# Optimization experiments

Hardware: AMD Instinct MI355X
Metric: run time of the kernel (lower is better)

Reference implementation:

```python
import jax, jax.numpy as jnp
import numpy as np

N = 50000
E = 1600000
N_INPUT, N_ENC1, N_ENC2, N_ENC3, N_Z, N_CLUSTERS = 512, 500, 500, 2000, 10, 10
SIGMA = 0.5


def _xavier(key, shape):
    bound = float(np.sqrt(6.0 / (shape[0] + shape[1])))
    return jax.random.uniform(key, shape, jnp.float32, -bound, bound)


def setup_inputs() -> dict:
    key = jax.random.key(0)
    ks = jax.random.split(key, 13)
    x = jax.random.normal(ks[0], (N, N_INPUT), jnp.float32)
    tra1 = jax.random.normal(ks[1], (N, N_ENC1), jnp.float32)
    tra2 = jax.random.normal(ks[2], (N, N_ENC2), jnp.float32)
    tra3 = jax.random.normal(ks[3], (N, N_ENC3), jnp.float32)
    z = jax.random.normal(ks[4], (N, N_Z), jnp.float32)
    edge_vals = jax.random.uniform(ks[5], (E,), jnp.float32)
    row = jax.random.randint(ks[6], (E,), 0, N, jnp.int32)
    col = jax.random.randint(ks[7], (E,), 0, N, jnp.int32)
    W1 = _xavier(ks[8], (N_INPUT, N_ENC1))
    W2 = _xavier(ks[9], (N_ENC1, N_ENC2))
    W3 = _xavier(ks[10], (N_ENC2, N_ENC3))
    W4 = _xavier(ks[11], (N_ENC3, N_Z))
    W5 = _xavier(ks[12], (N_Z, N_CLUSTERS))
    return {"x": x, "tra1": tra1, "tra2": tra2, "tra3": tra3, "z": z,
            "edge_vals": edge_vals, "row": row, "col": col,
            "W1": W1, "W2": W2, "W3": W3, "W4": W4, "W5": W5}


def _spmm(row, col, vals, m):
    # out[i] = sum_{e: row[e]==i} vals[e] * m[col[e]]  (sparse adj @ m)
    return jax.ops.segment_sum(vals[:, None] * m[col], row, num_segments=N)


def _gnn_layer(feats, W, row, col, vals, active=True):
    out = _spmm(row, col, vals, feats @ W)
    return jax.nn.relu(out) if active else out


def reference(x, tra1, tra2, tra3, z, edge_vals, row, col, W1, W2, W3, W4, W5):
    s = SIGMA
    h = _gnn_layer(x, W1, row, col, edge_vals)
    h = _gnn_layer((1 - s) * h + s * tra1, W2, row, col, edge_vals)
    h = _gnn_layer((1 - s) * h + s * tra2, W3, row, col, edge_vals)
    h = _gnn_layer((1 - s) * h + s * tra3, W4, row, col, edge_vals)
    h = _gnn_layer((1 - s) * h + s * z, W5, row, col, edge_vals, active=False)
    return jax.nn.softmax(h, axis=1)
```

## Files before the change

### kernel.cpp

```cpp
#include <hip/hip_runtime.h>
#include <cstddef>
#include <cstdint>


constexpr int D_IN = 512;
constexpr int D1   = 500;
constexpr int D2   = 500;
constexpr int D3   = 2000;
constexpr int DC   = 10;

__global__ void zero_i32(int* __restrict__ p, int n) {
    int i = blockIdx.x * 256 + threadIdx.x;
    if (i < n) p[i] = 0;
}

__global__ void count_edges(const int* __restrict__ row, int E, int* __restrict__ cnt) {
    int e = blockIdx.x * 256 + threadIdx.x;
    if (e < E) atomicAdd(&cnt[row[e]], 1);
}

__global__ __launch_bounds__(1024) void scan_rowptr(const int* __restrict__ cnt, int Nr,
                                                    int* __restrict__ rp, int* __restrict__ cur) {
    __shared__ int sb[1024];
    const int t = threadIdx.x;
    int carry = 0;
    for (int base = 0; base < Nr; base += 1024) {
        int idx = base + t;
        int c = (idx < Nr) ? cnt[idx] : 0;
        sb[t] = c;
        __syncthreads();
        for (int off = 1; off < 1024; off <<= 1) {
            int add = (t >= off) ? sb[t - off] : 0;
            __syncthreads();
            sb[t] += add;
            __syncthreads();
        }
        if (idx < Nr) { int ex = carry + sb[t] - c; rp[idx] = ex; cur[idx] = ex; }
        carry += sb[1023];
        __syncthreads();
    }
    if (t == 0) rp[Nr] = carry;
}

__global__ void scatter_edges(const int* __restrict__ row, const int* __restrict__ col,
                              const float* __restrict__ val, int E,
                              int* __restrict__ cur, int* __restrict__ ci,
                              float* __restrict__ cv) {
    int e = blockIdx.x * 256 + threadIdx.x;
    if (e < E) {
        int r = row[e];
        int p = atomicAdd(&cur[r], 1);
        ci[p] = col[e];
        cv[p] = val[e];
    }
}

constexpr int BM = 64, BN = 64, BK = 16;

__global__ __launch_bounds__(256) void gemm_tiled(const float* __restrict__ A,
                                                  const float* __restrict__ B,
                                                  float* __restrict__ C,
                                                  int M, int K, int Nn) {
    __shared__ float As[BM][BK + 1];
    __shared__ float Bs[BK][BN];
    const int tid = threadIdx.x;
    const int tx = tid & 15, ty = tid >> 4;
    const int rowBase = blockIdx.y * BM, colBase = blockIdx.x * BN;
    float acc[4][4] = {};
    for (int k0 = 0; k0 < K; k0 += BK) {
        for (int e = tid; e < BM * BK; e += 256) {
            int m = e >> 4, k = e & 15;
            int gr = rowBase + m, gk = k0 + k;
            As[m][k] = (gr < M && gk < K) ? A[(size_t)gr * K + gk] : 0.f;
        }
        for (int e = tid; e < BK * BN; e += 256) {
            int k = e >> 6, n = e & 63;
            int gk = k0 + k, gc = colBase + n;
            Bs[k][n] = (gk < K && gc < Nn) ? B[(size_t)gk * Nn + gc] : 0.f;
        }
        __syncthreads();
        for (int k = 0; k < BK; k++) {
            float a[4], b[4];
#pragma unroll
            for (int i = 0; i < 4; i++) a[i] = As[ty * 4 + i][k];
#pragma unroll
            for (int j = 0; j < 4; j++) b[j] = Bs[k][tx * 4 + j];
#pragma unroll
            for (int i = 0; i < 4; i++)
#pragma unroll
                for (int j = 0; j < 4; j++) acc[i][j] += a[i] * b[j];
        }
        __syncthreads();
    }
#pragma unroll
    for (int i = 0; i < 4; i++) {
        int gr = rowBase + ty * 4 + i;
        if (gr >= M) continue;
#pragma unroll
        for (int j = 0; j < 4; j++) {
            int gc = colBase + tx * 4 + j;
            if (gc < Nn) C[(size_t)gr * Nn + gc] = acc[i][j];
        }
    }
}

constexpr int R3  = 20;
constexpr int JB  = 256;

__global__ __launch_bounds__(256, 3) void gemm34(const float* __restrict__ g3,
                                                 const float* __restrict__ W3,
                                                 const float* __restrict__ W4,
                                                 float* __restrict__ t4) {
    __shared__ float gs[R3 * D2];
    const int t = threadIdx.x;
    const size_t i0 = (size_t)blockIdx.x * R3;

    {
        const float4* src = reinterpret_cast<const float4*>(g3 + i0 * D2);
        float4* dst = reinterpret_cast<float4*>(gs);
        for (int e = t; e < R3 * D2 / 4; e += 256) dst[e] = src[e];
    }
    __syncthreads();

    const int lane = t & 63;
    const int rb = (t >> 6) * 5;
    float acc[5][10] = {};

    for (int j0 = 0; j0 < D3; j0 += JB) {
        const int jb = min(JB, D3 - j0);
        const int j4 = lane * 4;
        if (j4 < jb) {
            float pacc[5][4] = {};
            const float* w3p = W3 + j0 + j4;
            float4 wa[4], wb[4];

            auto load_w3 = [&](float4 (&dst)[4], int k) {
#pragma unroll
                for (int kk = 0; kk < 4; kk++)
                    dst[kk] = *reinterpret_cast<const float4*>(w3p + (k + kk) * D3);
            };
            auto fma_grp = [&](const float4 (&wv)[4], int k) {
                float4 ga[5];
#pragma unroll
                for (int i = 0; i < 5; i++)
                    ga[i] = *reinterpret_cast<const float4*>(&gs[(rb + i) * D2 + k]);
#pragma unroll
                for (int kk = 0; kk < 4; kk++)
#pragma unroll
                    for (int i = 0; i < 5; i++) {
                        const float av = reinterpret_cast<const float*>(&ga[i])[kk];
#pragma unroll
                        for (int jj = 0; jj < 4; jj++)
                            pacc[i][jj] += av * reinterpret_cast<const float*>(&wv[kk])[jj];
                    }
            };

            load_w3(wa, 0);
            for (int k = 0; k < D2 - 4; k += 8) {
                load_w3(wb, k + 4);
                fma_grp(wa, k);
                load_w3(wa, k + 8);
                fma_grp(wb, k + 4);
            }
            fma_grp(wa, D2 - 4);

#pragma unroll
            for (int jj = 0; jj < 4; jj++) {
                const float* w4r = W4 + (j0 + j4 + jj) * DC;
                float w4v[10];
#pragma unroll
                for (int h = 0; h < 5; h++) {
                    float2 u = *reinterpret_cast<const float2*>(w4r + 2 * h);
                    w4v[2 * h] = u.x;
                    w4v[2 * h + 1] = u.y;
                }
#pragma unroll
                for (int i = 0; i < 5; i++) {
                    const float p = fmaxf(pacc[i][jj], 0.f);
#pragma unroll
                    for (int c = 0; c < 10; c++) acc[i][c] += p * w4v[c];
                }
            }
        }
    }

#pragma unroll
    for (int i = 0; i < 5; i++)
#pragma unroll
        for (int c = 0; c < 10; c++) {
            float v = acc[i][c];
            v += __shfl_xor(v, 1, 64);
            v += __shfl_xor(v, 2, 64);
            v += __shfl_xor(v, 4, 64);
            v += __shfl_xor(v, 8, 64);
            v += __shfl_xor(v, 16, 64);
            v += __shfl_xor(v, 32, 64);
            acc[i][c] = v;
        }
    if (lane == 0) {
        float* dst = t4 + (i0 + rb) * DC;
#pragma unroll
        for (int i = 0; i < 5; i++)
#pragma unroll
            for (int c = 0; c < 10; c++) dst[i * DC + c] = 0.5f * acc[i][c];
    }
}

constexpr int RT = 16;

__global__ __launch_bounds__(256) void tra3w4(const float* __restrict__ tra3,
                                              const float* __restrict__ W4,
                                              float* __restrict__ t4) {
    const int t = threadIdx.x;
    const int r = t >> 4, l = t & 15;
    const size_t i = (size_t)blockIdx.x * RT + r;
    const float* rowp = tra3 + i * D3;
    float a[10] = {};
    for (int m = l; m < D3 / 4; m += 16) {
        float4 v = *reinterpret_cast<const float4*>(rowp + m * 4);
        const float* w4r = W4 + m * 4 * DC;
        const float vv[4] = {v.x, v.y, v.z, v.w};
#pragma unroll
        for (int q = 0; q < 4; q++)
#pragma unroll
            for (int c = 0; c < 10; c++) a[c] += vv[q] * w4r[q * DC + c];
    }
#pragma unroll
    for (int c = 0; c < 10; c++) {
        float v = a[c];
        v += __shfl_xor(v, 1, 64);
        v += __shfl_xor(v, 2, 64);
        v += __shfl_xor(v, 4, 64);
        v += __shfl_xor(v, 8, 64);
        a[c] = v;
    }
    if (l == 0) {
        float* dst = t4 + i * DC;
#pragma unroll
        for (int c = 0; c < 10; c++) dst[c] += 0.5f * a[c];
    }
}

__global__ __launch_bounds__(256) void spmm_w(const int* __restrict__ rp,
                                              const int* __restrict__ ci,
                                              const float* __restrict__ cv,
                                              const float* __restrict__ m,
                                              float* __restrict__ out,
                                              const float* __restrict__ mix,
                                              int relu) {
    const int i = blockIdx.x, t = threadIdx.x;
    const int c0 = t, c1 = t + 256;
    float a0 = 0.f, a1 = 0.f;
    const int pb = rp[i], pe = rp[i + 1];
    for (int p = pb; p < pe; p++) {
        const int col = ci[p];
        const float v = cv[p];
        const float* mr = m + (size_t)col * D1;
        a0 += v * mr[c0];
        if (c1 < D1) a1 += v * mr[c1];
    }
    if (relu) { a0 = fmaxf(a0, 0.f); a1 = fmaxf(a1, 0.f); }
    const size_t o = (size_t)i * D1;
    if (mix) {
        out[o + c0] = 0.5f * a0 + 0.5f * mix[o + c0];
        if (c1 < D1) out[o + c1] = 0.5f * a1 + 0.5f * mix[o + c1];
    } else {
        out[o + c0] = a0;
        if (c1 < D1) out[o + c1] = a1;
    }
}

__global__ __launch_bounds__(256) void spmm_n(const int* __restrict__ rp,
                                              const int* __restrict__ ci,
                                              const float* __restrict__ cv,
                                              const float* __restrict__ m,
                                              float* __restrict__ out,
                                              const float* __restrict__ mix,
                                              int relu, int Nr) {
    const int t = threadIdx.x;
    const int lr = t / DC, c = t - lr * DC;
    if (lr >= 25) return;
    const int i = blockIdx.x * 25 + lr;
    if (i >= Nr) return;
    float a = 0.f;
    const int pb = rp[i], pe = rp[i + 1];
    for (int p = pb; p < pe; p++) a += cv[p] * m[(size_t)ci[p] * DC + c];
    if (relu) a = fmaxf(a, 0.f);
    if (mix) a = 0.5f * a + 0.5f * mix[(size_t)i * DC + c];
    out[(size_t)i * DC + c] = a;
}

__global__ void softmax10(const float* __restrict__ in, float* __restrict__ out, int Nr) {
    int i = blockIdx.x * 256 + threadIdx.x;
    if (i >= Nr) return;
    const float* r = in + (size_t)i * DC;
    float v[DC], mx = r[0];
#pragma unroll
    for (int c = 0; c < DC; c++) { v[c] = r[c]; mx = fmaxf(mx, v[c]); }
    float s = 0.f;
#pragma unroll
    for (int c = 0; c < DC; c++) { v[c] = __expf(v[c] - mx); s += v[c]; }
    float inv = 1.0f / s;
    float* o = out + (size_t)i * DC;
#pragma unroll
    for (int c = 0; c < DC; c++) o[c] = v[c] * inv;
}

extern "C" void kernel_launch(void* const* d_in, const int* in_sizes, int n_in,
                              void* d_out, int out_size, void* d_ws, size_t ws_size,
                              hipStream_t stream) {
    const float* x    = (const float*)d_in[0];
    const float* tra1 = (const float*)d_in[1];
    const float* tra2 = (const float*)d_in[2];
    const float* tra3 = (const float*)d_in[3];
    const float* z    = (const float*)d_in[4];
    const float* ev   = (const float*)d_in[5];
    const int*   erow = (const int*)d_in[6];
    const int*   ecol = (const int*)d_in[7];
    const float* W1   = (const float*)d_in[8];
    const float* W2   = (const float*)d_in[9];
    const float* W3   = (const float*)d_in[10];
    const float* W4   = (const float*)d_in[11];
    const float* W5   = (const float*)d_in[12];

    const int Nr = in_sizes[4] / DC;
    const int E  = in_sizes[5];

    char* ws = (char*)d_ws;
    size_t off = 0;
    auto alloc = [&](size_t bytes) -> char* {
        char* p = ws + off;
        off = (off + bytes + 255) & ~(size_t)255;
        return p;
    };
    float* B0  = (float*)alloc((size_t)Nr * D1 * 4);
    float* B1  = (float*)alloc((size_t)Nr * D1 * 4);
    float* t4  = (float*)alloc((size_t)Nr * DC * 4);
    float* a4  = (float*)alloc((size_t)Nr * DC * 4);
    float* g5  = (float*)alloc((size_t)Nr * DC * 4);
    float* pre = (float*)alloc((size_t)Nr * DC * 4);
    int*   rp  = (int*)alloc((size_t)(Nr + 1) * 4);
    int*   cur = (int*)alloc((size_t)Nr * 4);
    int*   cnt = (int*)alloc((size_t)Nr * 4);
    int*   ci  = (int*)alloc((size_t)E * 4);
    float* cv  = (float*)alloc((size_t)E * 4);

    const int eb = (E + 255) / 256;
    const int nb = (Nr + 255) / 256;

    zero_i32<<<nb, 256, 0, stream>>>(cnt, Nr);
    count_edges<<<eb, 256, 0, stream>>>(erow, E, cnt);
    scan_rowptr<<<1, 1024, 0, stream>>>(cnt, Nr, rp, cur);
    scatter_edges<<<eb, 256, 0, stream>>>(erow, ecol, ev, E, cur, ci, cv);

    auto gg = [&](int M, int Nn) { return dim3((Nn + BN - 1) / BN, (M + BM - 1) / BM); };

    gemm_tiled<<<gg(Nr, D1), 256, 0, stream>>>(x, W1, B0, Nr, D_IN, D1);
    spmm_w<<<Nr, 256, 0, stream>>>(rp, ci, cv, B0, B1, tra1, 1);
    gemm_tiled<<<gg(Nr, D2), 256, 0, stream>>>(B1, W2, B0, Nr, D1, D2);
    spmm_w<<<Nr, 256, 0, stream>>>(rp, ci, cv, B0, B1, tra2, 1);
    spmm_w<<<Nr, 256, 0, stream>>>(rp, ci, cv, B1, B0, nullptr, 0);
    gemm34<<<Nr / R3, 256, 0, stream>>>(B0, W3, W4, t4);
    tra3w4<<<Nr / RT, 256, 0, stream>>>(tra3, W4, t4);
    spmm_n<<<(Nr + 24) / 25, 256, 0, stream>>>(rp, ci, cv, t4, a4, z, 1, Nr);
    gemm_tiled<<<gg(Nr, DC), 256, 0, stream>>>(a4, W5, g5, Nr, DC, DC);
    spmm_n<<<(Nr + 24) / 25, 256, 0, stream>>>(rp, ci, cv, g5, pre, nullptr, 0, Nr);
    softmax10<<<nb, 256, 0, stream>>>(pre, (float*)d_out, Nr);
}
```

Before: 5.438 ms.

## Replace tiled GEMMs with row-stripe GEMM staging weight k-slabs in shared memory

```diff
diff --git a/kernel.cpp b/kernel.cpp
--- a/kernel.cpp
+++ b/kernel.cpp
@@ -8,6 +8,9 @@
 constexpr int D2   = 500;
 constexpr int D3   = 2000;
 constexpr int DC   = 10;
+
+constexpr int RS = 32;
+constexpr int KG = 16;
 
 __global__ void zero_i32(int* __restrict__ p, int n) {
     int i = blockIdx.x * 256 + threadIdx.x;
@@ -55,154 +58,213 @@
     }
 }
 
-constexpr int BM = 64, BN = 64, BK = 16;
-
-__global__ __launch_bounds__(256) void gemm_tiled(const float* __restrict__ A,
-                                                  const float* __restrict__ B,
-                                                  float* __restrict__ C,
-                                                  int M, int K, int Nn) {
-    __shared__ float As[BM][BK + 1];
-    __shared__ float Bs[BK][BN];
-    const int tid = threadIdx.x;
-    const int tx = tid & 15, ty = tid >> 4;
-    const int rowBase = blockIdx.y * BM, colBase = blockIdx.x * BN;
-    float acc[4][4] = {};
-    for (int k0 = 0; k0 < K; k0 += BK) {
-        for (int e = tid; e < BM * BK; e += 256) {
-            int m = e >> 4, k = e & 15;
-            int gr = rowBase + m, gk = k0 + k;
-            As[m][k] = (gr < M && gk < K) ? A[(size_t)gr * K + gk] : 0.f;
-        }
-        for (int e = tid; e < BK * BN; e += 256) {
-            int k = e >> 6, n = e & 63;
-            int gk = k0 + k, gc = colBase + n;
-            Bs[k][n] = (gk < K && gc < Nn) ? B[(size_t)gk * Nn + gc] : 0.f;
+__global__ __launch_bounds__(256, 4) void gemm_stripe(const float* __restrict__ A,
+                                                      const float* __restrict__ B,
+                                                      float* __restrict__ C,
+                                                      int M, int K, int Nn,
+                                                      const float* __restrict__ zpad) {
+    __shared__ float Ws[KG][512];
+    const int t = threadIdx.x;
+    const int lane = t & 63;
+    const int wid = t >> 6;
+    const int i0 = blockIdx.x * RS;
+    const int rb = wid * 8;
+
+    const float* Ar[8];
+#pragma unroll
+    for (int i = 0; i < 8; i++) {
+        int rg = i0 + rb + i;
+        rg = rg < M ? rg : M - 1;
+        Ar[i] = A + (size_t)rg * K;
+    }
+
+    float pacc[8][8] = {};
+    const int ngroups = (K + KG - 1) / KG;
+
+    for (int g = 0; g < ngroups; g++) {
+        const int k0 = g * KG;
+        const int kg = min(KG, K - k0);
+        float4 st[8];
+#pragma unroll
+        for (int q = 0; q < 8; q++) {
+            int e = t + 256 * q;
+            int kk = e >> 7, jj4 = (e & 127) << 2;
+            const float* src = (kk < kg && jj4 < Nn)
+                                   ? (B + (size_t)(k0 + kk) * Nn + jj4)
+                                   : zpad;
+            st[q] = *reinterpret_cast<const float4*>(src);
         }
         __syncthreads();
-        for (int k = 0; k < BK; k++) {
-            float a[4], b[4];
-#pragma unroll
-            for (int i = 0; i < 4; i++) a[i] = As[ty * 4 + i][k];
-#pragma unroll
-            for (int j = 0; j < 4; j++) b[j] = Bs[k][tx * 4 + j];
-#pragma unroll
-            for (int i = 0; i < 4; i++)
-#pragma unroll
-                for (int j = 0; j < 4; j++) acc[i][j] += a[i] * b[j];
+#pragma unroll
+        for (int q = 0; q < 8; q++) {
+            int e = t + 256 * q;
+            int kk = e >> 7, jj4 = (e & 127) << 2;
+            *reinterpret_cast<float4*>(&Ws[kk][jj4]) = st[q];
         }
         __syncthreads();
-    }
-#pragma unroll
-    for (int i = 0; i < 4; i++) {
-        int gr = rowBase + ty * 4 + i;
-        if (gr >= M) continue;
-#pragma unroll
-        for (int j = 0; j < 4; j++) {
-            int gc = colBase + tx * 4 + j;
-            if (gc < Nn) C[(size_t)gr * Nn + gc] = acc[i][j];
-        }
-    }
-}
-
-constexpr int R3  = 20;
-constexpr int JB  = 256;
-
-__global__ __launch_bounds__(256, 3) void gemm34(const float* __restrict__ g3,
+        for (int k4 = 0; k4 < kg; k4 += 4) {
+            float4 ga[8];
+#pragma unroll
+            for (int i = 0; i < 8; i++)
+                ga[i] = *reinterpret_cast<const float4*>(Ar[i] + k0 + k4);
+#pragma unroll
+            for (int q = 0; q < 4; q++) {
+                float4 wlo = *reinterpret_cast<const float4*>(&Ws[k4 + q][4 * lane]);
+                float4 whi = *reinterpret_cast<const float4*>(&Ws[k4 + q][256 + 4 * lane]);
+#pragma unroll
+                for (int i = 0; i < 8; i++) {
+                    const float av = reinterpret_cast<const float*>(&ga[i])[q];
+                    pacc[i][0] += av * wlo.x;
+                    pacc[i][1] += av * wlo.y;
+                    pacc[i][2] += av * wlo.z;
+                    pacc[i][3] += av * wlo.w;
+                    pacc[i][4] += av * whi.x;
+                    pacc[i][5] += av * whi.y;
+                    pacc[i][6] += av * whi.z;
+                    pacc[i][7] += av * whi.w;
+                }
+            }
+        }
+    }
+#pragma unroll
+    for (int i = 0; i < 8; i++) {
+        int row = i0 + rb + i;
+        if (row >= M) break;
+        if (4 * lane + 4 <= Nn) {
+            float4 lo;
+            lo.x = pacc[i][0]; lo.y = pacc[i][1]; lo.z = pacc[i][2]; lo.w = pacc[i][3];
+            *reinterpret_cast<float4*>(C + (size_t)row * Nn + 4 * lane) = lo;
+        }
+        if (260 + 4 * lane <= Nn) {
+            float4 hi;
+            hi.x = pacc[i][4]; hi.y = pacc[i][5]; hi.z = pacc[i][6]; hi.w = pacc[i][7];
+            *reinterpret_cast<float4*>(C + (size_t)row * Nn + 256 + 4 * lane) = hi;
+        }
+    }
+}
+
+__global__ __launch_bounds__(256, 4) void gemm34(const float* __restrict__ g3,
                                                  const float* __restrict__ W3,
                                                  const float* __restrict__ W4,
-                                                 float* __restrict__ t4) {
-    __shared__ float gs[R3 * D2];
-    const int t = threadIdx.x;
-    const size_t i0 = (size_t)blockIdx.x * R3;
-
-    {
-        const float4* src = reinterpret_cast<const float4*>(g3 + i0 * D2);
-        float4* dst = reinterpret_cast<float4*>(gs);
-        for (int e = t; e < R3 * D2 / 4; e += 256) dst[e] = src[e];
-    }
-    __syncthreads();
-
+                                                 float* __restrict__ t4,
+                                                 int M, const float* __restrict__ zpad) {
+    __shared__ float Ws[KG][512];
+    const int t = threadIdx.x;
     const int lane = t & 63;
-    const int rb = (t >> 6) * 5;
-    float acc[5][10] = {};
-
-    for (int j0 = 0; j0 < D3; j0 += JB) {
-        const int jb = min(JB, D3 - j0);
-        const int j4 = lane * 4;
-        if (j4 < jb) {
-            float pacc[5][4] = {};
-            const float* w3p = W3 + j0 + j4;
-            float4 wa[4], wb[4];
-
-            auto load_w3 = [&](float4 (&dst)[4], int k) {
-#pragma unroll
-                for (int kk = 0; kk < 4; kk++)
-                    dst[kk] = *reinterpret_cast<const float4*>(w3p + (k + kk) * D3);
-            };
-            auto fma_grp = [&](const float4 (&wv)[4], int k) {
-                float4 ga[5];
-#pragma unroll
-                for (int i = 0; i < 5; i++)
-                    ga[i] = *reinterpret_cast<const float4*>(&gs[(rb + i) * D2 + k]);
-#pragma unroll
-                for (int kk = 0; kk < 4; kk++)
-#pragma unroll
-                    for (int i = 0; i < 5; i++) {
-                        const float av = reinterpret_cast<const float*>(&ga[i])[kk];
-#pragma unroll
-                        for (int jj = 0; jj < 4; jj++)
-                            pacc[i][jj] += av * reinterpret_cast<const float*>(&wv[kk])[jj];
+    const int wid = t >> 6;
+    const int i0 = blockIdx.x * RS;
+    const int rb = wid * 8;
+
+    const float* Ar[8];
+#pragma unroll
+    for (int i = 0; i < 8; i++) {
+        int rg = i0 + rb + i;
+        rg = rg < M ? rg : M - 1;
+        Ar[i] = g3 + (size_t)rg * D2;
+    }
+
+    for (int j0 = 0; j0 < D3; j0 += 512) {
+        float pacc[8][8] = {};
+        const int ngroups = (D2 + KG - 1) / KG;
+        for (int g = 0; g < ngroups; g++) {
+            const int k0 = g * KG;
+            const int kg = min(KG, D2 - k0);
+            float4 st[8];
+#pragma unroll
+            for (int q = 0; q < 8; q++) {
+                int e = t + 256 * q;
+                int kk = e >> 7, jj4 = (e & 127) << 2;
+                const float* src = (kk < kg && j0 + jj4 < D3)
+                                       ? (W3 + (size_t)(k0 + kk) * D3 + j0 + jj4)
+                                       : zpad;
+                st[q] = *reinterpret_cast<const float4*>(src);
+            }
+            __syncthreads();
+#pragma unroll
+            for (int q = 0; q < 8; q++) {
+                int e = t + 256 * q;
+                int kk = e >> 7, jj4 = (e & 127) << 2;
+                *reinterpret_cast<float4*>(&Ws[kk][jj4]) = st[q];
+            }
+            __syncthreads();
+            for (int k4 = 0; k4 < kg; k4 += 4) {
+                float4 ga[8];
+#pragma unroll
+                for (int i = 0; i < 8; i++)
+                    ga[i] = *reinterpret_cast<const float4*>(Ar[i] + k0 + k4);
+#pragma unroll
+                for (int q = 0; q < 4; q++) {
+                    float4 wlo = *reinterpret_cast<const float4*>(&Ws[k4 + q][4 * lane]);
+                    float4 whi = *reinterpret_cast<const float4*>(&Ws[k4 + q][256 + 4 * lane]);
+#pragma unroll
+                    for (int i = 0; i < 8; i++) {
+                        const float av = reinterpret_cast<const float*>(&ga[i])[q];
+                        pacc[i][0] += av * wlo.x;
+                        pacc[i][1] += av * wlo.y;
+                        pacc[i][2] += av * wlo.z;
+                        pacc[i][3] += av * wlo.w;
+                        pacc[i][4] += av * whi.x;
+                        pacc[i][5] += av * whi.y;
+                        pacc[i][6] += av * whi.z;
+                        pacc[i][7] += av * whi.w;
                     }
-            };
-
-            load_w3(wa, 0);
-            for (int k = 0; k < D2 - 4; k += 8) {
-                load_w3(wb, k + 4);
-                fma_grp(wa, k);
-                load_w3(wa, k + 8);
-                fma_grp(wb, k + 4);
-            }
-            fma_grp(wa, D2 - 4);
-
-#pragma unroll
-            for (int jj = 0; jj < 4; jj++) {
-                const float* w4r = W4 + (j0 + j4 + jj) * DC;
-                float w4v[10];
-#pragma unroll
-                for (int h = 0; h < 5; h++) {
-                    float2 u = *reinterpret_cast<const float2*>(w4r + 2 * h);
-                    w4v[2 * h] = u.x;
-                    w4v[2 * h + 1] = u.y;
                 }
-#pragma unroll
-                for (int i = 0; i < 5; i++) {
-                    const float p = fmaxf(pacc[i][jj], 0.f);
-#pragma unroll
-                    for (int c = 0; c < 10; c++) acc[i][c] += p * w4v[c];
+            }
+        }
+#pragma unroll
+        for (int h = 0; h < 2; h++) {
+            float ea[4][10] = {};
+#pragma unroll
+            for (int s = 0; s < 2; s++) {
+#pragma unroll
+                for (int jj = 0; jj < 4; jj++) {
+                    const int jc = j0 + s * 256 + 4 * lane + jj;
+                    float w4v[10];
+                    if (jc < D3) {
+                        const float* w4r = W4 + (size_t)jc * DC;
+#pragma unroll
+                        for (int u = 0; u < 5; u++) {
+                            float2 f = *reinterpret_cast<const float2*>(w4r + 2 * u);
+                            w4v[2 * u] = f.x;
+                            w4v[2 * u + 1] = f.y;
+                        }
+                    } else {
+#pragma unroll
+                        for (int c = 0; c < 10; c++) w4v[c] = 0.f;
+                    }
+#pragma unroll
+                    for (int i = 0; i < 4; i++) {
+                        const float p = fmaxf(pacc[h * 4 + i][s * 4 + jj], 0.f);
+#pragma unroll
+                        for (int c = 0; c < 10; c++) ea[i][c] += p * w4v[c];
+                    }
                 }
             }
-        }
-    }
-
-#pragma unroll
-    for (int i = 0; i < 5; i++)
-#pragma unroll
-        for (int c = 0; c < 10; c++) {
-            float v = acc[i][c];
-            v += __shfl_xor(v, 1, 64);
-            v += __shfl_xor(v, 2, 64);
-            v += __shfl_xor(v, 4, 64);
-            v += __shfl_xor(v, 8, 64);
-            v += __shfl_xor(v, 16, 64);
-            v += __shfl_xor(v, 32, 64);
-            acc[i][c] = v;
-        }
-    if (lane == 0) {
-        float* dst = t4 + (i0 + rb) * DC;
-#pragma unroll
-        for (int i = 0; i < 5; i++)
-#pragma unroll
-            for (int c = 0; c < 10; c++) dst[i * DC + c] = 0.5f * acc[i][c];
+#pragma unroll
+            for (int i = 0; i < 4; i++)
+#pragma unroll
+                for (int c = 0; c < 10; c++) {
+                    float v = ea[i][c];
+                    v += __shfl_xor(v, 1, 64);
+                    v += __shfl_xor(v, 2, 64);
+                    v += __shfl_xor(v, 4, 64);
+                    v += __shfl_xor(v, 8, 64);
+                    v += __shfl_xor(v, 16, 64);
+                    v += __shfl_xor(v, 32, 64);
+                    ea[i][c] = v;
+                }
+            if (lane == 0) {
+#pragma unroll
+                for (int i = 0; i < 4; i++) {
+                    const int row = i0 + rb + h * 4 + i;
+                    if (row < M) {
+                        float* dst = t4 + (size_t)row * DC;
+#pragma unroll
+                        for (int c = 0; c < 10; c++) dst[c] += 0.5f * ea[i][c];
+                    }
+                }
+            }
+        }
     }
 }
 
@@ -237,7 +299,39 @@
     if (l == 0) {
         float* dst = t4 + i * DC;
 #pragma unroll
-        for (int c = 0; c < 10; c++) dst[c] += 0.5f * a[c];
+        for (int c = 0; c < 10; c++) dst[c] = 0.5f * a[c];
+    }
+}
+
+__global__ __launch_bounds__(256) void gemm10(const float* __restrict__ a4,
+                                              const float* __restrict__ W5,
+                                              float* __restrict__ g5, int Nr) {
+    __shared__ float w5s[DC * DC];
+    const int t = threadIdx.x;
+    if (t < DC * DC) w5s[t] = W5[t];
+    __syncthreads();
+    const int i = blockIdx.x * 256 + t;
+    if (i >= Nr) return;
+    const float* ar = a4 + (size_t)i * DC;
+    float a[DC];
+#pragma unroll
+    for (int u = 0; u < 5; u++) {
+        float2 f = *reinterpret_cast<const float2*>(ar + 2 * u);
+        a[2 * u] = f.x;
+        a[2 * u + 1] = f.y;
+    }
+    float o[DC] = {};
+#pragma unroll
+    for (int k = 0; k < DC; k++)
+#pragma unroll
+        for (int c = 0; c < DC; c++) o[c] += a[k] * w5s[k * DC + c];
+    float* dst = g5 + (size_t)i * DC;
+#pragma unroll
+    for (int u = 0; u < 5; u++) {
+        float2 f;
+        f.x = o[2 * u];
+        f.y = o[2 * u + 1];
+        *reinterpret_cast<float2*>(dst + 2 * u) = f;
     }
 }
 
@@ -333,37 +427,39 @@
         off = (off + bytes + 255) & ~(size_t)255;
         return p;
     };
-    float* B0  = (float*)alloc((size_t)Nr * D1 * 4);
-    float* B1  = (float*)alloc((size_t)Nr * D1 * 4);
-    float* t4  = (float*)alloc((size_t)Nr * DC * 4);
-    float* a4  = (float*)alloc((size_t)Nr * DC * 4);
-    float* g5  = (float*)alloc((size_t)Nr * DC * 4);
-    float* pre = (float*)alloc((size_t)Nr * DC * 4);
-    int*   rp  = (int*)alloc((size_t)(Nr + 1) * 4);
-    int*   cur = (int*)alloc((size_t)Nr * 4);
-    int*   cnt = (int*)alloc((size_t)Nr * 4);
-    int*   ci  = (int*)alloc((size_t)E * 4);
-    float* cv  = (float*)alloc((size_t)E * 4);
+    float* B0   = (float*)alloc((size_t)Nr * D1 * 4);
+    float* B1   = (float*)alloc((size_t)Nr * D1 * 4);
+    float* t4   = (float*)alloc((size_t)Nr * DC * 4);
+    float* a4   = (float*)alloc((size_t)Nr * DC * 4);
+    float* g5   = (float*)alloc((size_t)Nr * DC * 4);
+    float* pre  = (float*)alloc((size_t)Nr * DC * 4);
+    int*   rp   = (int*)alloc((size_t)(Nr + 1) * 4);
+    int*   cur  = (int*)alloc((size_t)Nr * 4);
+    int*   cnt  = (int*)alloc((size_t)Nr * 4);
+    int*   ci   = (int*)alloc((size_t)E * 4);
+    float* cv   = (float*)alloc((size_t)E * 4);
+    float* zpad = (float*)alloc(256);
 
     const int eb = (E + 255) / 256;
     const int nb = (Nr + 255) / 256;
+    const int gsb = (Nr + RS - 1) / RS;
 
     zero_i32<<<nb, 256, 0, stream>>>(cnt, Nr);
+    zero_i32<<<1, 256, 0, stream>>>((int*)zpad, 64);
     count_edges<<<eb, 256, 0, stream>>>(erow, E, cnt);
     scan_rowptr<<<1, 1024, 0, stream>>>(cnt, Nr, rp, cur);
     scatter_edges<<<eb, 256, 0, stream>>>(erow, ecol, ev, E, cur, ci, cv);
 
-    auto gg = [&](int M, int Nn) { return dim3((Nn + BN - 1) / BN, (M + BM - 1) / BM); };
-
-    gemm_tiled<<<gg(Nr, D1), 256, 0, stream>>>(x, W1, B0, Nr, D_IN, D1);
+    tra3w4<<<Nr / RT, 256, 0, stream>>>(tra3, W4, t4);
+
+    gemm_stripe<<<gsb, 256, 0, stream>>>(x, W1, B0, Nr, D_IN, D1, zpad);
     spmm_w<<<Nr, 256, 0, stream>>>(rp, ci, cv, B0, B1, tra1, 1);
-    gemm_tiled<<<gg(Nr, D2), 256, 0, stream>>>(B1, W2, B0, Nr, D1, D2);
+    gemm_stripe<<<gsb, 256, 0, stream>>>(B1, W2, B0, Nr, D1, D2, zpad);
     spmm_w<<<Nr, 256, 0, stream>>>(rp, ci, cv, B0, B1, tra2, 1);
     spmm_w<<<Nr, 256, 0, stream>>>(rp, ci, cv, B1, B0, nullptr, 0);
-    gemm34<<<Nr / R3, 256, 0, stream>>>(B0, W3, W4, t4);
-    tra3w4<<<Nr / RT, 256, 0, stream>>>(tra3, W4, t4);
+    gemm34<<<gsb, 256, 0, stream>>>(B0, W3, W4, t4, Nr, zpad);
     spmm_n<<<(Nr + 24) / 25, 256, 0, stream>>>(rp, ci, cv, t4, a4, z, 1, Nr);
-    gemm_tiled<<<gg(Nr, DC), 256, 0, stream>>>(a4, W5, g5, Nr, DC, DC);
+    gemm10<<<nb, 256, 0, stream>>>(a4, W5, g5, Nr);
     spmm_n<<<(Nr + 24) / 25, 256, 0, stream>>>(rp, ci, cv, g5, pre, nullptr, 0, Nr);
     softmax10<<<nb, 256, 0, stream>>>(pre, (float*)d_out, Nr);
 }
```

After: 9.575 ms. +76.1%, slower.

## Restructure fused W3/W4 GEMM to tile 20 rows per wave with column chunks

Applied to the files above, without the earlier changes.

```diff
diff --git a/kernel.cpp b/kernel.cpp
--- a/kernel.cpp
+++ b/kernel.cpp
@@ -104,105 +104,96 @@
     }
 }
 
-constexpr int R3  = 20;
-constexpr int JB  = 256;
-
-__global__ __launch_bounds__(256, 3) void gemm34(const float* __restrict__ g3,
-                                                 const float* __restrict__ W3,
-                                                 const float* __restrict__ W4,
-                                                 float* __restrict__ t4) {
-    __shared__ float gs[R3 * D2];
-    const int t = threadIdx.x;
-    const size_t i0 = (size_t)blockIdx.x * R3;
-
-    {
-        const float4* src = reinterpret_cast<const float4*>(g3 + i0 * D2);
-        float4* dst = reinterpret_cast<float4*>(gs);
-        for (int e = t; e < R3 * D2 / 4; e += 256) dst[e] = src[e];
-    }
-    __syncthreads();
-
+constexpr int RB = 20;
+
+__global__ __launch_bounds__(256) void gemm34(const float* __restrict__ g3,
+                                              const float* __restrict__ W3,
+                                              const float* __restrict__ W4,
+                                              float* __restrict__ t4) {
+    __shared__ float part[4][RB][DC];
+    const int t = threadIdx.x;
     const int lane = t & 63;
-    const int rb = (t >> 6) * 5;
-    float acc[5][10] = {};
-
-    for (int j0 = 0; j0 < D3; j0 += JB) {
-        const int jb = min(JB, D3 - j0);
-        const int j4 = lane * 4;
-        if (j4 < jb) {
-            float pacc[5][4] = {};
-            const float* w3p = W3 + j0 + j4;
-            float4 wa[4], wb[4];
-
-            auto load_w3 = [&](float4 (&dst)[4], int k) {
-#pragma unroll
-                for (int kk = 0; kk < 4; kk++)
-                    dst[kk] = *reinterpret_cast<const float4*>(w3p + (k + kk) * D3);
-            };
-            auto fma_grp = [&](const float4 (&wv)[4], int k) {
-                float4 ga[5];
-#pragma unroll
-                for (int i = 0; i < 5; i++)
-                    ga[i] = *reinterpret_cast<const float4*>(&gs[(rb + i) * D2 + k]);
-#pragma unroll
-                for (int kk = 0; kk < 4; kk++)
-#pragma unroll
-                    for (int i = 0; i < 5; i++) {
-                        const float av = reinterpret_cast<const float*>(&ga[i])[kk];
-#pragma unroll
-                        for (int jj = 0; jj < 4; jj++)
-                            pacc[i][jj] += av * reinterpret_cast<const float*>(&wv[kk])[jj];
-                    }
-            };
-
-            load_w3(wa, 0);
-            for (int k = 0; k < D2 - 4; k += 8) {
-                load_w3(wb, k + 4);
-                fma_grp(wa, k);
-                load_w3(wa, k + 8);
-                fma_grp(wb, k + 4);
+    const int wid = t >> 6;
+    const int i0 = blockIdx.x * RB;
+    const float* rowbase = g3 + (size_t)i0 * D2;
+
+    for (int e = lane; e < RB * DC; e += 64) part[wid][e / DC][e % DC] = 0.f;
+
+    for (int cc = 0; cc < 2; cc++) {
+        const int chunk = wid + 4 * cc;
+        const int j4 = chunk * 256 + 4 * lane;
+        const float* w3p = W3 + j4;
+        float pacc[RB][4] = {};
+
+        float4 wa0, wa1, wb0, wb1;
+        auto load_a = [&](float4& d0, float4& d1, int k) {
+            d0 = *reinterpret_cast<const float4*>(w3p + (size_t)k * D3);
+            d1 = *reinterpret_cast<const float4*>(w3p + (size_t)(k + 1) * D3);
+        };
+        auto fma_grp = [&](const float4& w0, const float4& w1, int k) {
+#pragma unroll
+            for (int i = 0; i < RB; i++) {
+                const float* ar = rowbase + (size_t)i * D2 + k;
+                const float a0 = ar[0], a1 = ar[1];
+                pacc[i][0] += a0 * w0.x; pacc[i][1] += a0 * w0.y;
+                pacc[i][2] += a0 * w0.z; pacc[i][3] += a0 * w0.w;
+                pacc[i][0] += a1 * w1.x; pacc[i][1] += a1 * w1.y;
+                pacc[i][2] += a1 * w1.z; pacc[i][3] += a1 * w1.w;
             }
-            fma_grp(wa, D2 - 4);
-
+        };
+
+        load_a(wa0, wa1, 0);
+        for (int k = 0; k < D2 - 4; k += 4) {
+            load_a(wb0, wb1, k + 2);
+            fma_grp(wa0, wa1, k);
+            load_a(wa0, wa1, k + 4);
+            fma_grp(wb0, wb1, k + 2);
+        }
+        load_a(wb0, wb1, D2 - 2);
+        fma_grp(wa0, wa1, D2 - 4);
+        fma_grp(wb0, wb1, D2 - 2);
+
+#pragma unroll
+        for (int qr = 0; qr < RB / 4; qr++) {
+            float ea[4][DC] = {};
 #pragma unroll
             for (int jj = 0; jj < 4; jj++) {
-                const float* w4r = W4 + (j0 + j4 + jj) * DC;
-                float w4v[10];
-#pragma unroll
-                for (int h = 0; h < 5; h++) {
-                    float2 u = *reinterpret_cast<const float2*>(w4r + 2 * h);
-                    w4v[2 * h] = u.x;
-                    w4v[2 * h + 1] = u.y;
+                const float* w4r = W4 + (size_t)(j4 + jj) * DC;
+                float w4v[DC];
+#pragma unroll
+                for (int u = 0; u < 5; u++) {
+                    float2 f = *reinterpret_cast<const float2*>(w4r + 2 * u);
+                    w4v[2 * u] = f.x;
+                    w4v[2 * u + 1] = f.y;
                 }
 #pragma unroll
-                for (int i = 0; i < 5; i++) {
-                    const float p = fmaxf(pacc[i][jj], 0.f);
-#pragma unroll
-                    for (int c = 0; c < 10; c++) acc[i][c] += p * w4v[c];
+                for (int i = 0; i < 4; i++) {
+                    const float p = fmaxf(pacc[qr * 4 + i][jj], 0.f);
+#pragma unroll
+                    for (int c = 0; c < DC; c++) ea[i][c] += p * w4v[c];
                 }
             }
-        }
-    }
-
-#pragma unroll
-    for (int i = 0; i < 5; i++)
-#pragma unroll
-        for (int c = 0; c < 10; c++) {
-            float v = acc[i][c];
-            v += __shfl_xor(v, 1, 64);
-            v += __shfl_xor(v, 2, 64);
-            v += __shfl_xor(v, 4, 64);
-            v += __shfl_xor(v, 8, 64);
-            v += __shfl_xor(v, 16, 64);
-            v += __shfl_xor(v, 32, 64);
-            acc[i][c] = v;
-        }
-    if (lane == 0) {
-        float* dst = t4 + (i0 + rb) * DC;
-#pragma unroll
-        for (int i = 0; i < 5; i++)
-#pragma unroll
-            for (int c = 0; c < 10; c++) dst[i * DC + c] = 0.5f * acc[i][c];
+#pragma unroll
+            for (int i = 0; i < 4; i++)
+#pragma unroll
+                for (int c = 0; c < DC; c++) {
+                    float v = ea[i][c];
+                    v += __shfl_xor(v, 1, 64);
+                    v += __shfl_xor(v, 2, 64);
+                    v += __shfl_xor(v, 4, 64);
+                    v += __shfl_xor(v, 8, 64);
+                    v += __shfl_xor(v, 16, 64);
+                    v += __shfl_xor(v, 32, 64);
+                    if (lane == c) part[wid][qr * 4 + i][c] += v;
+                }
+        }
+    }
+
+    __syncthreads();
+    for (int e = t; e < RB * DC; e += 256) {
+        const int r = e / DC, c = e - r * DC;
+        float s = part[0][r][c] + part[1][r][c] + part[2][r][c] + part[3][r][c];
+        t4[(size_t)(i0 + r) * DC + c] += 0.5f * s;
     }
 }
 
@@ -237,7 +228,39 @@
     if (l == 0) {
         float* dst = t4 + i * DC;
 #pragma unroll
-        for (int c = 0; c < 10; c++) dst[c] += 0.5f * a[c];
+        for (int c = 0; c < 10; c++) dst[c] = 0.5f * a[c];
+    }
+}
+
+__global__ __launch_bounds__(256) void gemm10(const float* __restrict__ a4,
+                                              const float* __restrict__ W5,
+                                              float* __restrict__ g5, int Nr) {
+    __shared__ float w5s[DC * DC];
+    const int t = threadIdx.x;
+    if (t < DC * DC) w5s[t] = W5[t];
+    __syncthreads();
+    const int i = blockIdx.x * 256 + t;
+    if (i >= Nr) return;
+    const float* ar = a4 + (size_t)i * DC;
+    float a[DC];
+#pragma unroll
+    for (int u = 0; u < 5; u++) {
+        float2 f = *reinterpret_cast<const float2*>(ar + 2 * u);
+        a[2 * u] = f.x;
+        a[2 * u + 1] = f.y;
+    }
+    float o[DC] = {};
+#pragma unroll
+    for (int k = 0; k < DC; k++)
+#pragma unroll
+        for (int c = 0; c < DC; c++) o[c] += a[k] * w5s[k * DC + c];
+    float* dst = g5 + (size_t)i * DC;
+#pragma unroll
+    for (int u = 0; u < 5; u++) {
+        float2 f;
+        f.x = o[2 * u];
+        f.y = o[2 * u + 1];
+        *reinterpret_cast<float2*>(dst + 2 * u) = f;
     }
 }
 
@@ -353,6 +376,8 @@
     scan_rowptr<<<1, 1024, 0, stream>>>(cnt, Nr, rp, cur);
     scatter_edges<<<eb, 256, 0, stream>>>(erow, ecol, ev, E, cur, ci, cv);
 
+    tra3w4<<<Nr / RT, 256, 0, stream>>>(tra3, W4, t4);
+
     auto gg = [&](int M, int Nn) { return dim3((Nn + BN - 1) / BN, (M + BM - 1) / BM); };
 
     gemm_tiled<<<gg(Nr, D1), 256, 0, stream>>>(x, W1, B0, Nr, D_IN, D1);
@@ -360,10 +385,9 @@
     gemm_tiled<<<gg(Nr, D2), 256, 0, stream>>>(B1, W2, B0, Nr, D1, D2);
     spmm_w<<<Nr, 256, 0, stream>>>(rp, ci, cv, B0, B1, tra2, 1);
     spmm_w<<<Nr, 256, 0, stream>>>(rp, ci, cv, B1, B0, nullptr, 0);
-    gemm34<<<Nr / R3, 256, 0, stream>>>(B0, W3, W4, t4);
-    tra3w4<<<Nr / RT, 256, 0, stream>>>(tra3, W4, t4);
+    gemm34<<<Nr / RB, 256, 0, stream>>>(B0, W3, W4, t4);
     spmm_n<<<(Nr + 24) / 25, 256, 0, stream>>>(rp, ci, cv, t4, a4, z, 1, Nr);
-    gemm_tiled<<<gg(Nr, DC), 256, 0, stream>>>(a4, W5, g5, Nr, DC, DC);
+    gemm10<<<nb, 256, 0, stream>>>(a4, W5, g5, Nr);
     spmm_n<<<(Nr + 24) / 25, 256, 0, stream>>>(rp, ci, cv, g5, pre, nullptr, 0, Nr);
     softmax10<<<nb, 256, 0, stream>>>(pre, (float*)d_out, Nr);
 }
```

Result: faster. 5.322 ms (-2.1%).
